# Kernel optimization log

Hardware: AMD Instinct MI355X
Metric: run time of the kernel (lower is better)

Reference implementation:

```python
import jax, jax.numpy as jnp
import numpy as np

DIM = 768
HEADS = 12
HD = DIM // HEADS
E = 8
R = 64
ALPHA = 128.0
LORA_SCALE = ALPHA / R  # 2.0
ENABLE_BITS = np.array([1.0, 0.0, 1.0], dtype=np.float32)  # LoRA on q and v slices of qkv


def setup_inputs() -> dict:
    key = jax.random.key(0)
    ks = jax.random.split(key, 8)
    x = jax.random.normal(ks[0], (2, 4096, DIM), jnp.float32)
    # base (frozen) weights, shared across experts; no biases (qkv_bias=False)
    Wqkv = jax.random.normal(ks[1], (3 * DIM, DIM), jnp.float32) * 0.02
    Wproj = jax.random.normal(ks[2], (DIM, DIM), jnp.float32) * 0.02
    # per-expert LoRA adapters. qkv: shared down-proj A, per-output-slice up-proj B,
    # masked by enable bits (q,k,v).
    Aqkv = jax.random.normal(ks[3], (E, R, DIM), jnp.float32) * 0.02
    Bqkv = jax.random.normal(ks[4], (E, 3, DIM, R), jnp.float32) * 0.02
    Bqkv = Bqkv * jnp.asarray(ENABLE_BITS)[None, :, None, None]
    Aproj = jax.random.normal(ks[5], (E, R, DIM), jnp.float32) * 0.02
    Bproj = jax.random.normal(ks[6], (E, DIM, R), jnp.float32) * 0.02
    expert_indices = np.arange(4, dtype=np.int64) % E  # static per-chunk routing
    chunk_sizes = np.array([1024, 1024, 1024, 1024], dtype=np.int64)
    return {"x": x, "Wqkv": Wqkv, "Aqkv": Aqkv, "Bqkv": Bqkv, "Wproj": Wproj,
            "Aproj": Aproj, "Bproj": Bproj, "expert_indices": expert_indices,
            "chunk_sizes": chunk_sizes}


def reference(x, Wqkv, Aqkv, Bqkv, Wproj, Aproj, Bproj, expert_indices, chunk_sizes):
    # chunk sizes / expert indices are static host-side routing metadata
    sizes = [int(c) for c in np.asarray(chunk_sizes)]
    eidx = [int(e) for e in np.asarray(expert_indices)]
    offs = np.concatenate([[0], np.cumsum(sizes)])
    B = x.shape[0]
    scale = HD ** -0.5
    last_k = None
    last_v = None
    outs = []
    for i, n in enumerate(sizes):
        xc = x[:, offs[i]:offs[i + 1]]            # [B, n, DIM]
        e = eidx[i]
        # LoRA-adapted qkv for this chunk's expert
        base = xc @ Wqkv.T                        # [B, n, 3*DIM]
        h = xc @ Aqkv[e].T                        # [B, n, R]
        delta = jnp.einsum('bnr,tdr->bntd', h, Bqkv[e]).reshape(B, n, 3 * DIM)
        qkv = (base + LORA_SCALE * delta).reshape(B, n, 3, HEADS, HD)
        qkv = qkv.transpose(2, 0, 3, 1, 4)        # [3, B, H, n, HD]
        q, k, v = qkv[0], qkv[1], qkv[2]
        if last_k is not None:                    # growing KV over chunks (chunk-causal)
            k = jnp.concatenate([last_k, k], axis=-2)
            v = jnp.concatenate([last_v, v], axis=-2)
        last_k, last_v = k, v
        attn = jax.nn.softmax(jnp.einsum('bhqd,bhkd->bhqk', q * scale, k), axis=-1)
        o = jnp.einsum('bhqk,bhkd->bhqd', attn, v)
        o = o.transpose(0, 2, 1, 3).reshape(B, n, DIM)
        # LoRA-adapted output projection for the same expert
        o = o @ Wproj.T + LORA_SCALE * ((o @ Aproj[e].T) @ Bproj[e].T)
        outs.append(o)
    return jnp.concatenate(outs, axis=1)          # [B, total, DIM]
```

## Files before the change

### kernel.cpp

```cpp
#include <hip/hip_runtime.h>
#include <hip/hip_bf16.h>
#include <math.h>

#define BATCH   2
#define SEQ     4096
#define DIMD    768
#define NHEADS  12
#define HDIM    64
#define RR      64
#define CHUNK   1024
#define NTOK    (BATCH * SEQ)
#define BHN     (BATCH * NHEADS)
#define KC2     2304
#define QSCALE  0.18033688011112042f

typedef __attribute__((ext_vector_type(8))) short short8;
typedef __attribute__((ext_vector_type(4))) float f32x4;

#define AS1 __attribute__((address_space(1)))
#define AS3 __attribute__((address_space(3)))

__device__ __forceinline__ void glds16(const void* g, void* l) {
    __builtin_amdgcn_global_load_lds((const AS1 unsigned int*)g,
                                     (AS3 unsigned int*)l, 16, 0, 0);
}

__device__ __forceinline__ unsigned pk2u(float a, float b) {
    float2 t; t.x = a; t.y = b;
    __hip_bfloat162 r = __float22bfloat162_rn(t);
    union { __hip_bfloat162 b2; unsigned u; } c; c.b2 = r;
    return c.u;
}
__device__ __forceinline__ float lo16f(unsigned p) { return __uint_as_float(p << 16); }
__device__ __forceinline__ float hi16f(unsigned p) { return __uint_as_float(p & 0xffff0000u); }

__global__ __launch_bounds__(256)
void combine_split(const float* __restrict__ Wq, const float* __restrict__ Aq,
                   const float* __restrict__ Bq, unsigned short* __restrict__ outq,
                   const float* __restrict__ Wp, const float* __restrict__ Ap,
                   const float* __restrict__ Bp, unsigned short* __restrict__ outp)
{
    const int zz = blockIdx.z;
    const int e = zz & 3;
    const bool proj = zz >= 4;
    const int NB = proj ? DIMD : 3 * DIMD;
    if (proj && blockIdx.x >= 12) return;
    const float* W = proj ? Wp : Wq;
    const float* A = proj ? Ap : Aq;
    const float* Bm = proj ? Bp : Bq;
    unsigned short* out = proj ? outp : outq;

    const int tid = threadIdx.x;
    const int ty = tid >> 4, tx = tid & 15;
    const int f0 = blockIdx.x * 64, d0 = blockIdx.y * 64;

    __shared__ float Bb[64][68];
    __shared__ float Aa[64][68];

    const float* Ae = A + (long)e * RR * DIMD;
    const float* Be = Bm + (long)e * NB * RR;

    const int lrow = tid >> 2, lc = (tid & 3) * 16;
    #pragma unroll
    for (int u = 0; u < 16; u += 4) {
        *(float4*)&Bb[lrow][lc + u] = *(const float4*)&Be[(long)(f0 + lrow) * RR + lc + u];
        *(float4*)&Aa[lrow][lc + u] = *(const float4*)&Ae[(long)lrow * DIMD + d0 + lc + u];
    }
    __syncthreads();

    float acc[4][4] = {};
    #pragma unroll 4
    for (int r = 0; r < RR; r++) {
        const float4 bv = *(float4*)&Aa[r][tx * 4];
        #pragma unroll
        for (int i = 0; i < 4; i++) {
            const float av = Bb[ty + 16 * i][r];
            acc[i][0] = fmaf(av, bv.x, acc[i][0]);
            acc[i][1] = fmaf(av, bv.y, acc[i][1]);
            acc[i][2] = fmaf(av, bv.z, acc[i][2]);
            acc[i][3] = fmaf(av, bv.w, acc[i][3]);
        }
    }

    #pragma unroll
    for (int i = 0; i < 4; i++) {
        const int f = f0 + ty + 16 * i;
        const int d = d0 + tx * 4;
        unsigned short* o = out + ((long)e * NB + f) * KC2 + d;
        const float4 wv = *(const float4*)&W[(long)f * DIMD + d];
        const float v0 = wv.x + 2.0f * acc[i][0];
        const float v1 = wv.y + 2.0f * acc[i][1];
        const float v2 = wv.z + 2.0f * acc[i][2];
        const float v3 = wv.w + 2.0f * acc[i][3];
        uint2 hp, lp;
        hp.x = pk2u(v0, v1);
        hp.y = pk2u(v2, v3);
        lp.x = pk2u(v0 - lo16f(hp.x), v1 - hi16f(hp.x));
        lp.y = pk2u(v2 - lo16f(hp.y), v3 - hi16f(hp.y));
        *(uint2*)&o[0]    = hp;
        *(uint2*)&o[768]  = lp;
        *(uint2*)&o[1536] = hp;
    }
}

__global__ __launch_bounds__(192)
void build_xa2(const float* __restrict__ X, unsigned short* __restrict__ out)
{
    const int tok = blockIdx.x;
    const int j = threadIdx.x * 4;
    const float* xr = X + (long)tok * DIMD;
    unsigned short* o = out + (long)tok * KC2;
    float4 v = *(const float4*)&xr[j];
    uint2 hp, lp;
    hp.x = pk2u(v.x, v.y);
    hp.y = pk2u(v.z, v.w);
    lp.x = pk2u(v.x - lo16f(hp.x), v.y - hi16f(hp.x));
    lp.y = pk2u(v.z - lo16f(hp.y), v.w - hi16f(hp.y));
    *(uint2*)&o[j] = hp;
    *(uint2*)&o[768 + j] = hp;
    *(uint2*)&o[1536 + j] = lp;
}

template<bool SWAP>
__device__ __forceinline__ void gemm_core(const unsigned short* __restrict__ Ap,
                                          const unsigned short* __restrict__ Bp,
                                          unsigned short* lA, unsigned short* lB,
                                          f32x4 acc[4][4])
{
    const int tid = threadIdx.x;
    const int lane = tid & 63;
    const int wave = tid >> 6;
    const int n = lane & 15;
    const int quad = lane >> 4;
    const int wm = wave & 1, wn = wave >> 1;

    long soff[4];
    const int sldsoff = wave * 1024;
    #pragma unroll
    for (int iss = 0; iss < 4; iss++) {
        const int g = iss * 256 + tid;
        const int row = g >> 3;
        const int gc = (g & 7) ^ (row & 7);
        soff[iss] = (long)row * KC2 + gc * 8;
    }

    for (int k0 = 0; k0 < KC2; k0 += 64) {
        __syncthreads();
        #pragma unroll
        for (int iss = 0; iss < 4; iss++) {
            glds16(Ap + soff[iss] + k0, (char*)lA + iss * 4096 + sldsoff);
            glds16(Bp + soff[iss] + k0, (char*)lB + iss * 4096 + sldsoff);
        }
        __builtin_amdgcn_s_waitcnt(0);
        __syncthreads();

        #pragma unroll
        for (int kk = 0; kk < 2; kk++) {
            const int kg = kk * 4;
            short8 af[4], bfr[4];
            #pragma unroll
            for (int mt = 0; mt < 4; mt++) {
                const int r = wm * 64 + mt * 16 + n;
                const int p2 = (kg + quad) ^ (r & 7);
                af[mt] = *(const short8*)&lA[r * 64 + p2 * 8];
            }
            #pragma unroll
            for (int nt = 0; nt < 4; nt++) {
                const int r = wn * 64 + nt * 16 + n;
                const int p2 = (kg + quad) ^ (r & 7);
                bfr[nt] = *(const short8*)&lB[r * 64 + p2 * 8];
            }
            #pragma unroll
            for (int mt = 0; mt < 4; mt++)
                #pragma unroll
                for (int nt = 0; nt < 4; nt++) {
                    if (SWAP)
                        acc[mt][nt] = __builtin_amdgcn_mfma_f32_16x16x32_bf16(
                            bfr[nt], af[mt], acc[mt][nt], 0, 0, 0);
                    else
                        acc[mt][nt] = __builtin_amdgcn_mfma_f32_16x16x32_bf16(
                            af[mt], bfr[nt], acc[mt][nt], 0, 0, 0);
                }
        }
    }
}

__global__ __launch_bounds__(256)
void qkv_gemm(const unsigned short* __restrict__ A, const unsigned short* __restrict__ B,
              unsigned short* __restrict__ qpl, unsigned short* __restrict__ kpl,
              unsigned short* __restrict__ vpl)
{
    __shared__ __align__(16) unsigned short lA[128 * 64];
    __shared__ __align__(16) unsigned short lB[128 * 64];

    const int tid = threadIdx.x;
    const int lane = tid & 63;
    const int wave = tid >> 6;
    const int n = lane & 15;
    const int quad = lane >> 4;
    const int wm = wave & 1, wn = wave >> 1;
    const int id = blockIdx.x;

    f32x4 acc[4][4];
    #pragma unroll
    for (int i = 0; i < 4; i++)
        #pragma unroll
        for (int j = 0; j < 4; j++)
            acc[i][j] = (f32x4){0.f, 0.f, 0.f, 0.f};

    if (id < 768) {
        const int xcd = id & 7, loc = id >> 3;
        const int p = xcd * 6 + (loc >> 4), ml = loc & 15;
        const int e = p / 12, nb = p - e * 12;
        const int mb = ((ml >> 3) << 5) + e * 8 + (ml & 7);
        const int m0 = mb * 128, n0 = nb * 128;
        gemm_core<true>(A + (long)m0 * KC2, B + ((long)e * 2304 + n0) * KC2, lA, lB, acc);
        #pragma unroll
        for (int mt = 0; mt < 4; mt++) {
            #pragma unroll
            for (int nt = 0; nt < 4; nt++) {
                f32x4 a = acc[mt][nt];
                const int fb = n0 + wn * 64 + nt * 16 + quad * 4;
                const int t = fb >= 768 ? 1 : 0;
                const int rem = fb - t * 768;
                const int head = rem >> 6;
                const int d0 = rem & 63;
                const int token = m0 + wm * 64 + mt * 16 + n;
                const int b = token >> 12, s = token & (SEQ - 1);
                const int bh = b * NHEADS + head;
                const float sc = t ? 1.0f : QSCALE;
                unsigned short* dst = (t ? kpl : qpl) + ((long)(bh * SEQ + s)) * HDIM + d0;
                uint2 pk;
                pk.x = pk2u(a[0] * sc, a[1] * sc);
                pk.y = pk2u(a[2] * sc, a[3] * sc);
                *(uint2*)dst = pk;
            }
        }
    } else {
        const int id2 = id - 768;
        const int xcd = id2 & 7, loc = id2 >> 3;
        const int p = xcd * 3 + (loc >> 4), ml = loc & 15;
        const int e = p / 6, nb = p - e * 6;
        const int mb = ((ml >> 3) << 5) + e * 8 + (ml & 7);
        const int m0 = mb * 128, n0 = 1536 + nb * 128;
        gemm_core<false>(A + (long)m0 * KC2, B + ((long)e * 2304 + n0) * KC2, lA, lB, acc);
        #pragma unroll
        for (int mt = 0; mt < 4; mt++) {
            #pragma unroll
            for (int nt = 0; nt < 4; nt++) {
                f32x4 a = acc[mt][nt];
                const int f = n0 + wn * 64 + nt * 16 + n;
                const int head = (f - 1536) >> 6;
                const int d = f & 63;
                const int tok0 = m0 + wm * 64 + mt * 16 + quad * 4;
                const int b = tok0 >> 12, s0 = tok0 & (SEQ - 1);
                const int bh = b * NHEADS + head;
                unsigned short* dst = vpl + ((long)(bh * HDIM + d)) * SEQ + s0;
                uint2 pk;
                pk.x = pk2u(a[0], a[1]);
                pk.y = pk2u(a[2], a[3]);
                *(uint2*)dst = pk;
            }
        }
    }
}

__global__ __launch_bounds__(256)
void proj_gemm(const unsigned short* __restrict__ A, const unsigned short* __restrict__ B,
               float* __restrict__ outf)
{
    __shared__ __align__(16) unsigned short lA[128 * 64];
    __shared__ __align__(16) unsigned short lB[128 * 64];

    const int tid = threadIdx.x;
    const int lane = tid & 63;
    const int wave = tid >> 6;
    const int n = lane & 15;
    const int quad = lane >> 4;
    const int wm = wave & 1, wn = wave >> 1;

    const int id = blockIdx.x;
    const int xcd = id & 7, loc = id >> 3;
    const int p = xcd * 3 + (loc >> 4), ml = loc & 15;
    const int e = p / 6, nb = p - e * 6;
    const int mb = ((ml >> 3) << 5) + e * 8 + (ml & 7);
    const int m0 = mb * 128, n0 = nb * 128;

    f32x4 acc[4][4];
    #pragma unroll
    for (int i = 0; i < 4; i++)
        #pragma unroll
        for (int j = 0; j < 4; j++)
            acc[i][j] = (f32x4){0.f, 0.f, 0.f, 0.f};

    gemm_core<true>(A + (long)m0 * KC2, B + ((long)e * 768 + n0) * KC2, lA, lB, acc);

    #pragma unroll
    for (int mt = 0; mt < 4; mt++)
        #pragma unroll
        for (int nt = 0; nt < 4; nt++) {
            const int fb = n0 + wn * 64 + nt * 16 + quad * 4;
            const int token = m0 + wm * 64 + mt * 16 + n;
            *(f32x4*)&outf[(long)token * DIMD + fb] = acc[mt][nt];
        }
}

__global__ __launch_bounds__(256)
void attn_split(const unsigned short* __restrict__ qp,
                const unsigned short* __restrict__ kpl,
                const unsigned short* __restrict__ vtp,
                unsigned short* __restrict__ XA,
                float* __restrict__ pO, float* __restrict__ pl)
{
    __shared__ __align__(16) unsigned short lK[64 * 64];
    __shared__ __align__(16) unsigned short lV[64 * 64];
    __shared__ __align__(16) unsigned short lP[4][64 * 64];

    const int tid = threadIdx.x;
    const int lane = tid & 63;
    const int wave = tid >> 6;
    const int n = lane & 15;
    const int quad = lane >> 4;
    const int c7 = n & 7;

    const int id = blockIdx.x;
    const int xcd = id & 7;
    const int loc = id >> 3;
    const int sub = loc % 3;
    const int r2 = loc / 3;
    const int z = r2 % 10;
    const int qb = r2 / 10;
    const int bh = xcd * 3 + sub;

    int ci, ks0, pidx;
    if (z < 4)      { ci = 3; ks0 = z * 1024;       pidx = z; }
    else if (z < 7) { ci = 2; ks0 = (z - 4) * 1024; pidx = z; }
    else if (z < 9) { ci = 1; ks0 = (z - 7) * 1024; pidx = z; }
    else            { ci = 0; ks0 = 0;              pidx = -1; }
    const int b = bh / NHEADS;
    const int h = bh - b * NHEADS;

    const long planeQK = (long)bh * SEQ * HDIM;
    const long planeVt = (long)bh * HDIM * SEQ;
    const int qch = qb * 256 + wave * 64;
    const int q0 = ci * CHUNK + qch;

    long skoff[2], svoff[2];
    #pragma unroll
    for (int p = 0; p < 2; p++) {
        const int g = p * 256 + tid;
        const int row = g >> 3;
        const int gc = (g & 7) ^ (row & 7);
        skoff[p] = (long)row * HDIM + gc * 8;
        svoff[p] = (long)row * SEQ + gc * 8;
    }

    short8 qf[4][2];
    #pragma unroll
    for (int qt = 0; qt < 4; qt++)
        #pragma unroll
        for (int s = 0; s < 2; s++)
            qf[qt][s] = *(const short8*)&qp[planeQK + (long)(q0 + qt * 16 + n) * HDIM + s * 32 + quad * 8];

    const short8 ones8 = {0x3f80, 0x3f80, 0x3f80, 0x3f80, 0x3f80, 0x3f80, 0x3f80, 0x3f80};

    f32x4 acc[4][4];
    f32x4 accl[4];
    #pragma unroll
    for (int m2 = 0; m2 < 4; m2++)
        #pragma unroll
        for (int qt = 0; qt < 4; qt++)
            acc[m2][qt] = (f32x4){0.f, 0.f, 0.f, 0.f};
    #pragma unroll
    for (int qt = 0; qt < 4; qt++) accl[qt] = (f32x4){0.f, 0.f, 0.f, 0.f};

    unsigned short* Pw = &lP[wave][0];

    for (int kt0 = 0; kt0 < 16; kt0++) {
        const int k0 = ks0 + kt0 * 64;
        __syncthreads();
        glds16(kpl + planeQK + (long)k0 * HDIM + skoff[0], (char*)lK + wave * 1024);
        glds16(kpl + planeQK + (long)k0 * HDIM + skoff[1], (char*)lK + 4096 + wave * 1024);
        glds16(vtp + planeVt + k0 + svoff[0], (char*)lV + wave * 1024);
        glds16(vtp + planeVt + k0 + svoff[1], (char*)lV + 4096 + wave * 1024);
        __builtin_amdgcn_s_waitcnt(0);
        __syncthreads();

        #pragma unroll
        for (int half = 0; half < 2; half++) {
            f32x4 st[4][2];
            #pragma unroll
            for (int kt = 0; kt < 4; kt++) {
                st[kt][0] = (f32x4){0.f, 0.f, 0.f, 0.f};
                st[kt][1] = (f32x4){0.f, 0.f, 0.f, 0.f};
            }
            #pragma unroll
            for (int s = 0; s < 2; s++) {
                #pragma unroll
                for (int kt = 0; kt < 4; kt++) {
                    const int gr = (s * 4 + quad) ^ c7;
                    short8 kf = *(const short8*)&lK[(kt * 16 + n) * 64 + gr * 8];
                    st[kt][0] = __builtin_amdgcn_mfma_f32_16x16x32_bf16(kf, qf[2 * half][s],     st[kt][0], 0, 0, 0);
                    st[kt][1] = __builtin_amdgcn_mfma_f32_16x16x32_bf16(kf, qf[2 * half + 1][s], st[kt][1], 0, 0, 0);
                }
            }
            #pragma unroll
            for (int q2 = 0; q2 < 2; q2++) {
                const int qt = 2 * half + q2;
                unsigned short* prow = Pw + (qt * 16 + n) * 64;
                #pragma unroll
                for (int kt = 0; kt < 4; kt++) {
                    uint2 pkv;
                    pkv.x = pk2u(__builtin_exp2f(st[kt][q2][0]), __builtin_exp2f(st[kt][q2][1]));
                    pkv.y = pk2u(__builtin_exp2f(st[kt][q2][2]), __builtin_exp2f(st[kt][q2][3]));
                    const int gsw = (2 * kt + (quad >> 1)) ^ c7;
                    *(uint2*)&prow[gsw * 8 + (quad & 1) * 4] = pkv;
                }
            }
        }

        #pragma unroll
        for (int hh = 0; hh < 2; hh++) {
            short8 pf[4];
            #pragma unroll
            for (int qt = 0; qt < 4; qt++) {
                const int gsw = (hh * 4 + quad) ^ c7;
                pf[qt] = *(const short8*)&Pw[(qt * 16 + n) * 64 + gsw * 8];
            }
            #pragma unroll
            for (int m2 = 0; m2 < 4; m2++) {
                const int gr = (hh * 4 + quad) ^ c7;
                short8 vf = *(const short8*)&lV[(m2 * 16 + n) * 64 + gr * 8];
                #pragma unroll
                for (int qt = 0; qt < 4; qt++)
                    acc[m2][qt] = __builtin_amdgcn_mfma_f32_16x16x32_bf16(vf, pf[qt], acc[m2][qt], 0, 0, 0);
            }
            #pragma unroll
            for (int qt = 0; qt < 4; qt++)
                accl[qt] = __builtin_amdgcn_mfma_f32_16x16x32_bf16(ones8, pf[qt], accl[qt], 0, 0, 0);
        }
    }

    if (pidx < 0) {
        #pragma unroll
        for (int qt = 0; qt < 4; qt++) {
            const float inv = 1.0f / accl[qt][0];
            const int token = b * SEQ + q0 + qt * 16 + n;
            unsigned short* xrow = XA + (long)token * KC2;
            #pragma unroll
            for (int m2 = 0; m2 < 4; m2++) {
                const int d = h * HDIM + m2 * 16 + quad * 4;
                const float o0 = acc[m2][qt][0] * inv;
                const float o1 = acc[m2][qt][1] * inv;
                const float o2 = acc[m2][qt][2] * inv;
                const float o3 = acc[m2][qt][3] * inv;
                uint2 hp, lp;
                hp.x = pk2u(o0, o1);
                hp.y = pk2u(o2, o3);
                lp.x = pk2u(o0 - lo16f(hp.x), o1 - hi16f(hp.x));
                lp.y = pk2u(o2 - lo16f(hp.y), o3 - hi16f(hp.y));
                *(uint2*)&xrow[d] = hp;
                *(uint2*)&xrow[768 + d] = hp;
                *(uint2*)&xrow[1536 + d] = lp;
            }
        }
    } else {
        const long pq = (long)(pidx * BHN + bh) * 1024 + qch;
        #pragma unroll
        for (int qt = 0; qt < 4; qt++) {
            const long qoff = (pq + qt * 16 + n) * 64;
            #pragma unroll
            for (int m2 = 0; m2 < 4; m2++)
                *(f32x4*)&pO[qoff + m2 * 16 + quad * 4] = acc[m2][qt];
            if (quad == 0)
                pl[pq + qt * 16 + n] = accl[qt][0];
        }
    }
}

__global__ __launch_bounds__(256)
void attn_combine(const float* __restrict__ pO, const float* __restrict__ pl,
                  unsigned short* __restrict__ XA)
{
    const int t = threadIdx.x;
    const int g = blockIdx.x;
    const int ci = 1 + (g >> 3);
    const int qb = g & 7;
    const int bh = blockIdx.y;
    const int b = bh / NHEADS, h = bh - b * NHEADS;
    const int pbase = (ci == 3) ? 0 : (ci == 2) ? 4 : 7;
    const int cnt = ci + 1;

    const int qrow = t >> 1;
    const int dh = (t & 1) * 32;
    const int qc = qb * 128 + qrow;

    float lsum = 0.f;
    for (int i = 0; i < cnt; i++)
        lsum += pl[(long)((pbase + i) * BHN + bh) * 1024 + qc];
    const float inv = 1.0f / lsum;
    const int token = b * SEQ + ci * CHUNK + qc;
    unsigned short* xrow = XA + (long)token * KC2 + h * HDIM + dh;

    #pragma unroll
    for (int u = 0; u < 8; u++) {
        float o0 = 0.f, o1 = 0.f, o2 = 0.f, o3 = 0.f;
        for (int i = 0; i < cnt; i++) {
            const long base = ((long)((pbase + i) * BHN + bh) * 1024 + qc) * 64 + dh + u * 4;
            const float4 a = *(const float4*)&pO[base];
            o0 += a.x; o1 += a.y; o2 += a.z; o3 += a.w;
        }
        o0 *= inv; o1 *= inv; o2 *= inv; o3 *= inv;
        uint2 hp, lp;
        hp.x = pk2u(o0, o1);
        hp.y = pk2u(o2, o3);
        lp.x = pk2u(o0 - lo16f(hp.x), o1 - hi16f(hp.x));
        lp.y = pk2u(o2 - lo16f(hp.y), o3 - hi16f(hp.y));
        *(uint2*)&xrow[u * 4] = hp;
        *(uint2*)&xrow[768 + u * 4] = hp;
        *(uint2*)&xrow[1536 + u * 4] = lp;
    }
}

extern "C" void kernel_launch(void* const* d_in, const int* in_sizes, int n_in,
                              void* d_out, int out_size, void* d_ws, size_t ws_size,
                              hipStream_t stream) {
    (void)in_sizes; (void)n_in; (void)out_size; (void)ws_size;
    const float* x     = (const float*)d_in[0];
    const float* Wqkv  = (const float*)d_in[1];
    const float* Aqkv  = (const float*)d_in[2];
    const float* Bqkv  = (const float*)d_in[3];
    const float* Wproj = (const float*)d_in[4];
    const float* Aproj = (const float*)d_in[5];
    const float* Bproj = (const float*)d_in[6];

    char* wsb = (char*)d_ws;
    unsigned short* XA   = (unsigned short*)(wsb);
    float*          pl   = (float*)(wsb + (36l << 20));
    unsigned short* qpl  = (unsigned short*)(wsb + (37l << 20));
    unsigned short* kpl  = (unsigned short*)(wsb + (50l << 20));
    unsigned short* vpl  = (unsigned short*)(wsb + (63l << 20));
    unsigned short* WBp  = (unsigned short*)(wsb + (76l << 20));
    unsigned short* WBq  = (unsigned short*)(wsb + (90l << 20));
    float*          pO   = (float*)(wsb + (90l << 20));

    dim3 blk(256);

    combine_split<<<dim3(36, 12, 8), blk, 0, stream>>>(
        Wqkv, Aqkv, Bqkv, WBq, Wproj, Aproj, Bproj, WBp);
    build_xa2<<<dim3(NTOK), dim3(192), 0, stream>>>(x, XA);
    qkv_gemm<<<dim3(1152), blk, 0, stream>>>(XA, WBq, qpl, kpl, vpl);
    attn_split<<<dim3(960), blk, 0, stream>>>(qpl, kpl, vpl, XA, pO, pl);
    attn_combine<<<dim3(24, BHN), blk, 0, stream>>>(pO, pl, XA);
    proj_gemm<<<dim3(384), blk, 0, stream>>>(XA, WBp, (float*)d_out);
}
```

Baseline: 510.6 us.

## Halve query and row tiles in attention and projection to double grid size

attn_split now gives each wave 32 queries instead of 64 and launches twice as many blocks. The K/V LDS fill is remapped per wave to match. proj_gemm drops from a 128x128 to a 64x128 output tile with its own inlined K loop, also doubling its block count. The aim is to fill the CUs better and cut tail imbalance on the small grids, at the cost of less K/V and weight reuse per block and more total global/LDS traffic.

```diff
diff --git a/kernel.cpp b/kernel.cpp
--- a/kernel.cpp
+++ b/kernel.cpp
@@ -269,7 +269,7 @@
 void proj_gemm(const unsigned short* __restrict__ A, const unsigned short* __restrict__ B,
                float* __restrict__ outf)
 {
-    __shared__ __align__(16) unsigned short lA[128 * 64];
+    __shared__ __align__(16) unsigned short lA[64 * 64];
     __shared__ __align__(16) unsigned short lB[128 * 64];
 
     const int tid = threadIdx.x;
@@ -281,26 +281,81 @@
 
     const int id = blockIdx.x;
     const int xcd = id & 7, loc = id >> 3;
-    const int p = xcd * 3 + (loc >> 4), ml = loc & 15;
+    const int p = xcd * 3 + (loc >> 5), ml = loc & 31;
     const int e = p / 6, nb = p - e * 6;
-    const int mb = ((ml >> 3) << 5) + e * 8 + (ml & 7);
-    const int m0 = mb * 128, n0 = nb * 128;
-
-    f32x4 acc[4][4];
-    #pragma unroll
-    for (int i = 0; i < 4; i++)
+    const int bb = ml >> 4, idx = ml & 15;
+    const int m0 = bb * SEQ + e * CHUNK + idx * 64;
+    const int n0 = nb * 128;
+
+    const unsigned short* Ap = A + (long)m0 * KC2;
+    const unsigned short* Bp = B + ((long)e * 768 + n0) * KC2;
+
+    long soffA[2], soffB[4];
+    const int sldsoff = wave * 1024;
+    #pragma unroll
+    for (int iss = 0; iss < 2; iss++) {
+        const int g = iss * 256 + tid;
+        const int row = g >> 3;
+        const int gc = (g & 7) ^ (row & 7);
+        soffA[iss] = (long)row * KC2 + gc * 8;
+    }
+    #pragma unroll
+    for (int iss = 0; iss < 4; iss++) {
+        const int g = iss * 256 + tid;
+        const int row = g >> 3;
+        const int gc = (g & 7) ^ (row & 7);
+        soffB[iss] = (long)row * KC2 + gc * 8;
+    }
+
+    f32x4 acc[2][4];
+    #pragma unroll
+    for (int i = 0; i < 2; i++)
         #pragma unroll
         for (int j = 0; j < 4; j++)
             acc[i][j] = (f32x4){0.f, 0.f, 0.f, 0.f};
 
-    gemm_core<true>(A + (long)m0 * KC2, B + ((long)e * 768 + n0) * KC2, lA, lB, acc);
-
-    #pragma unroll
-    for (int mt = 0; mt < 4; mt++)
+    for (int k0 = 0; k0 < KC2; k0 += 64) {
+        __syncthreads();
+        #pragma unroll
+        for (int iss = 0; iss < 2; iss++)
+            glds16(Ap + soffA[iss] + k0, (char*)lA + iss * 4096 + sldsoff);
+        #pragma unroll
+        for (int iss = 0; iss < 4; iss++)
+            glds16(Bp + soffB[iss] + k0, (char*)lB + iss * 4096 + sldsoff);
+        __builtin_amdgcn_s_waitcnt(0);
+        __syncthreads();
+
+        #pragma unroll
+        for (int kk = 0; kk < 2; kk++) {
+            const int kg = kk * 4;
+            short8 af[2], bfr[4];
+            #pragma unroll
+            for (int mt = 0; mt < 2; mt++) {
+                const int r = wm * 32 + mt * 16 + n;
+                const int p2 = (kg + quad) ^ (r & 7);
+                af[mt] = *(const short8*)&lA[r * 64 + p2 * 8];
+            }
+            #pragma unroll
+            for (int nt = 0; nt < 4; nt++) {
+                const int r = wn * 64 + nt * 16 + n;
+                const int p2 = (kg + quad) ^ (r & 7);
+                bfr[nt] = *(const short8*)&lB[r * 64 + p2 * 8];
+            }
+            #pragma unroll
+            for (int mt = 0; mt < 2; mt++)
+                #pragma unroll
+                for (int nt = 0; nt < 4; nt++)
+                    acc[mt][nt] = __builtin_amdgcn_mfma_f32_16x16x32_bf16(
+                        bfr[nt], af[mt], acc[mt][nt], 0, 0, 0);
+        }
+    }
+
+    #pragma unroll
+    for (int mt = 0; mt < 2; mt++)
         #pragma unroll
         for (int nt = 0; nt < 4; nt++) {
             const int fb = n0 + wn * 64 + nt * 16 + quad * 4;
-            const int token = m0 + wm * 64 + mt * 16 + n;
+            const int token = m0 + wm * 32 + mt * 16 + n;
             *(f32x4*)&outf[(long)token * DIMD + fb] = acc[mt][nt];
         }
 }
@@ -314,7 +369,7 @@
 {
     __shared__ __align__(16) unsigned short lK[64 * 64];
     __shared__ __align__(16) unsigned short lV[64 * 64];
-    __shared__ __align__(16) unsigned short lP[4][64 * 64];
+    __shared__ __align__(16) unsigned short lP[4][32 * 64];
 
     const int tid = threadIdx.x;
     const int lane = tid & 63;
@@ -342,88 +397,85 @@
 
     const long planeQK = (long)bh * SEQ * HDIM;
     const long planeVt = (long)bh * HDIM * SEQ;
-    const int qch = qb * 256 + wave * 64;
+    const int qch = qb * 128 + wave * 32;
     const int q0 = ci * CHUNK + qch;
 
     long skoff[2], svoff[2];
     #pragma unroll
     for (int p = 0; p < 2; p++) {
-        const int g = p * 256 + tid;
+        const int g = (wave * 2 + p) * 64 + lane;
         const int row = g >> 3;
         const int gc = (g & 7) ^ (row & 7);
         skoff[p] = (long)row * HDIM + gc * 8;
         svoff[p] = (long)row * SEQ + gc * 8;
     }
 
-    short8 qf[4][2];
-    #pragma unroll
-    for (int qt = 0; qt < 4; qt++)
+    short8 qf[2][2];
+    #pragma unroll
+    for (int qt = 0; qt < 2; qt++)
         #pragma unroll
         for (int s = 0; s < 2; s++)
             qf[qt][s] = *(const short8*)&qp[planeQK + (long)(q0 + qt * 16 + n) * HDIM + s * 32 + quad * 8];
 
     const short8 ones8 = {0x3f80, 0x3f80, 0x3f80, 0x3f80, 0x3f80, 0x3f80, 0x3f80, 0x3f80};
 
-    f32x4 acc[4][4];
-    f32x4 accl[4];
-    #pragma unroll
-    for (int m2 = 0; m2 < 4; m2++)
-        #pragma unroll
-        for (int qt = 0; qt < 4; qt++)
-            acc[m2][qt] = (f32x4){0.f, 0.f, 0.f, 0.f};
-    #pragma unroll
-    for (int qt = 0; qt < 4; qt++) accl[qt] = (f32x4){0.f, 0.f, 0.f, 0.f};
+    f32x4 acc[4][2];
+    f32x4 accl[2];
+    #pragma unroll
+    for (int m2 = 0; m2 < 4; m2++) {
+        acc[m2][0] = (f32x4){0.f, 0.f, 0.f, 0.f};
+        acc[m2][1] = (f32x4){0.f, 0.f, 0.f, 0.f};
+    }
+    accl[0] = (f32x4){0.f, 0.f, 0.f, 0.f};
+    accl[1] = (f32x4){0.f, 0.f, 0.f, 0.f};
 
     unsigned short* Pw = &lP[wave][0];
 
     for (int kt0 = 0; kt0 < 16; kt0++) {
         const int k0 = ks0 + kt0 * 64;
         __syncthreads();
-        glds16(kpl + planeQK + (long)k0 * HDIM + skoff[0], (char*)lK + wave * 1024);
-        glds16(kpl + planeQK + (long)k0 * HDIM + skoff[1], (char*)lK + 4096 + wave * 1024);
-        glds16(vtp + planeVt + k0 + svoff[0], (char*)lV + wave * 1024);
-        glds16(vtp + planeVt + k0 + svoff[1], (char*)lV + 4096 + wave * 1024);
+        glds16(kpl + planeQK + (long)k0 * HDIM + skoff[0], (char*)lK + wave * 2048);
+        glds16(kpl + planeQK + (long)k0 * HDIM + skoff[1], (char*)lK + wave * 2048 + 1024);
+        glds16(vtp + planeVt + k0 + svoff[0], (char*)lV + wave * 2048);
+        glds16(vtp + planeVt + k0 + svoff[1], (char*)lV + wave * 2048 + 1024);
         __builtin_amdgcn_s_waitcnt(0);
         __syncthreads();
 
-        #pragma unroll
-        for (int half = 0; half < 2; half++) {
-            f32x4 st[4][2];
+        f32x4 st[4][2];
+        #pragma unroll
+        for (int kt = 0; kt < 4; kt++) {
+            st[kt][0] = (f32x4){0.f, 0.f, 0.f, 0.f};
+            st[kt][1] = (f32x4){0.f, 0.f, 0.f, 0.f};
+        }
+        #pragma unroll
+        for (int s = 0; s < 2; s++) {
             #pragma unroll
             for (int kt = 0; kt < 4; kt++) {
-                st[kt][0] = (f32x4){0.f, 0.f, 0.f, 0.f};
-                st[kt][1] = (f32x4){0.f, 0.f, 0.f, 0.f};
-            }
-            #pragma unroll
-            for (int s = 0; s < 2; s++) {
-                #pragma unroll
-                for (int kt = 0; kt < 4; kt++) {
-                    const int gr = (s * 4 + quad) ^ c7;
-                    short8 kf = *(const short8*)&lK[(kt * 16 + n) * 64 + gr * 8];
-                    st[kt][0] = __builtin_amdgcn_mfma_f32_16x16x32_bf16(kf, qf[2 * half][s],     st[kt][0], 0, 0, 0);
-                    st[kt][1] = __builtin_amdgcn_mfma_f32_16x16x32_bf16(kf, qf[2 * half + 1][s], st[kt][1], 0, 0, 0);
-                }
-            }
-            #pragma unroll
-            for (int q2 = 0; q2 < 2; q2++) {
-                const int qt = 2 * half + q2;
-                unsigned short* prow = Pw + (qt * 16 + n) * 64;
-                #pragma unroll
-                for (int kt = 0; kt < 4; kt++) {
-                    uint2 pkv;
-                    pkv.x = pk2u(__builtin_exp2f(st[kt][q2][0]), __builtin_exp2f(st[kt][q2][1]));
-                    pkv.y = pk2u(__builtin_exp2f(st[kt][q2][2]), __builtin_exp2f(st[kt][q2][3]));
-                    const int gsw = (2 * kt + (quad >> 1)) ^ c7;
-                    *(uint2*)&prow[gsw * 8 + (quad & 1) * 4] = pkv;
-                }
+                const int gr = (s * 4 + quad) ^ c7;
+                short8 kf = *(const short8*)&lK[(kt * 16 + n) * 64 + gr * 8];
+                st[kt][0] = __builtin_amdgcn_mfma_f32_16x16x32_bf16(kf, qf[0][s], st[kt][0], 0, 0, 0);
+                st[kt][1] = __builtin_amdgcn_mfma_f32_16x16x32_bf16(kf, qf[1][s], st[kt][1], 0, 0, 0);
+            }
+        }
+
+        #pragma unroll
+        for (int qt = 0; qt < 2; qt++) {
+            unsigned short* prow = Pw + (qt * 16 + n) * 64;
+            #pragma unroll
+            for (int kt = 0; kt < 4; kt++) {
+                uint2 pkv;
+                pkv.x = pk2u(__builtin_exp2f(st[kt][qt][0]), __builtin_exp2f(st[kt][qt][1]));
+                pkv.y = pk2u(__builtin_exp2f(st[kt][qt][2]), __builtin_exp2f(st[kt][qt][3]));
+                const int gsw = (2 * kt + (quad >> 1)) ^ c7;
+                *(uint2*)&prow[gsw * 8 + (quad & 1) * 4] = pkv;
             }
         }
 
         #pragma unroll
         for (int hh = 0; hh < 2; hh++) {
-            short8 pf[4];
-            #pragma unroll
-            for (int qt = 0; qt < 4; qt++) {
+            short8 pf[2];
+            #pragma unroll
+            for (int qt = 0; qt < 2; qt++) {
                 const int gsw = (hh * 4 + quad) ^ c7;
                 pf[qt] = *(const short8*)&Pw[(qt * 16 + n) * 64 + gsw * 8];
             }
@@ -431,19 +483,17 @@
             for (int m2 = 0; m2 < 4; m2++) {
                 const int gr = (hh * 4 + quad) ^ c7;
                 short8 vf = *(const short8*)&lV[(m2 * 16 + n) * 64 + gr * 8];
-                #pragma unroll
-                for (int qt = 0; qt < 4; qt++)
-                    acc[m2][qt] = __builtin_amdgcn_mfma_f32_16x16x32_bf16(vf, pf[qt], acc[m2][qt], 0, 0, 0);
-            }
-            #pragma unroll
-            for (int qt = 0; qt < 4; qt++)
-                accl[qt] = __builtin_amdgcn_mfma_f32_16x16x32_bf16(ones8, pf[qt], accl[qt], 0, 0, 0);
+                acc[m2][0] = __builtin_amdgcn_mfma_f32_16x16x32_bf16(vf, pf[0], acc[m2][0], 0, 0, 0);
+                acc[m2][1] = __builtin_amdgcn_mfma_f32_16x16x32_bf16(vf, pf[1], acc[m2][1], 0, 0, 0);
+            }
+            accl[0] = __builtin_amdgcn_mfma_f32_16x16x32_bf16(ones8, pf[0], accl[0], 0, 0, 0);
+            accl[1] = __builtin_amdgcn_mfma_f32_16x16x32_bf16(ones8, pf[1], accl[1], 0, 0, 0);
         }
     }
 
     if (pidx < 0) {
         #pragma unroll
-        for (int qt = 0; qt < 4; qt++) {
+        for (int qt = 0; qt < 2; qt++) {
             const float inv = 1.0f / accl[qt][0];
             const int token = b * SEQ + q0 + qt * 16 + n;
             unsigned short* xrow = XA + (long)token * KC2;
@@ -467,7 +517,7 @@
     } else {
         const long pq = (long)(pidx * BHN + bh) * 1024 + qch;
         #pragma unroll
-        for (int qt = 0; qt < 4; qt++) {
+        for (int qt = 0; qt < 2; qt++) {
             const long qoff = (pq + qt * 16 + n) * 64;
             #pragma unroll
             for (int m2 = 0; m2 < 4; m2++)
@@ -550,7 +600,7 @@
         Wqkv, Aqkv, Bqkv, WBq, Wproj, Aproj, Bproj, WBp);
     build_xa2<<<dim3(NTOK), dim3(192), 0, stream>>>(x, XA);
     qkv_gemm<<<dim3(1152), blk, 0, stream>>>(XA, WBq, qpl, kpl, vpl);
-    attn_split<<<dim3(960), blk, 0, stream>>>(qpl, kpl, vpl, XA, pO, pl);
+    attn_split<<<dim3(1920), blk, 0, stream>>>(qpl, kpl, vpl, XA, pO, pl);
     attn_combine<<<dim3(24, BHN), blk, 0, stream>>>(pO, pl, XA);
-    proj_gemm<<<dim3(384), blk, 0, stream>>>(XA, WBp, (float*)d_out);
-}
+    proj_gemm<<<dim3(768), blk, 0, stream>>>(XA, WBp, (float*)d_out);
+}
```

New measurement: 476.6 us. 6.6% less time.
